# Performance work log

Hardware: AMD Instinct MI355X
Metric: run time of the kernel (lower is better)

The kernel has to match this reference:

```python
import jax, jax.numpy as jnp
import numpy as np

N_NODES = 100000
N_EDGES = 1600000
IN_DIM = 128
OUT_DIM = 32
HEADS = 4
EDGE_DIM = 32
N_ETYPES = 8
NEG_SLOPE = 0.2


def setup_inputs() -> dict:
    key = jax.random.key(0)
    ks = jax.random.split(key, 12)
    return {
        "h": jax.random.normal(ks[0], (N_NODES, IN_DIM), jnp.float32),
        "row": jax.random.randint(ks[1], (N_EDGES,), 0, N_NODES),
        "col": jax.random.randint(ks[2], (N_EDGES,), 0, N_NODES),
        "etype": jax.random.randint(ks[3], (N_EDGES,), 0, N_ETYPES),
        "edge_emb": jax.random.normal(ks[4], (N_ETYPES, EDGE_DIM), jnp.float32),
        "W": jax.random.normal(ks[5], (IN_DIM, OUT_DIM * HEADS), jnp.float32) * 0.1,
        "W_r_w": jax.random.normal(ks[6], (N_ETYPES, EDGE_DIM, EDGE_DIM * HEADS), jnp.float32) * 0.1,
        "a_l": jax.random.normal(ks[7], (1, HEADS, OUT_DIM), jnp.float32) * 0.1,
        "a_r": jax.random.normal(ks[8], (1, HEADS, OUT_DIM), jnp.float32) * 0.1,
        "a_e": jax.random.normal(ks[9], (1, HEADS, EDGE_DIM), jnp.float32) * 0.1,
        "res_w": jax.random.normal(ks[10], (IN_DIM, OUT_DIM * HEADS), jnp.float32) * 0.1,
        "res_b": jax.random.normal(ks[11], (OUT_DIM * HEADS,), jnp.float32) * 0.1,
    }


def reference(h, row, col, etype, edge_emb, W, W_r_w, a_l, a_r, a_e, res_w, res_b):
    N = h.shape[0]
    # node projection: (N, heads, out_dim)
    emb = (h @ W).reshape(N, HEADS, OUT_DIM)
    # TypedLinear on per-etype embeddings: compute once per etype, gather per edge
    typed = jnp.einsum('te,teo->to', edge_emb, W_r_w).reshape(N_ETYPES, HEADS, EDGE_DIM)
    e_emb = typed[etype]                                   # (E, heads, edge_dim)
    # attention logits
    h_l = jnp.sum(a_l * emb, axis=-1)                      # (N, heads)
    h_r = jnp.sum(a_r * emb, axis=-1)                      # (N, heads)
    h_e = jnp.sum(a_e * e_emb, axis=-1)                    # (E, heads)
    logits = jax.nn.leaky_relu(h_l[row] + h_r[col] + h_e, NEG_SLOPE)
    # edge softmax over incoming edges of each destination node (col)
    m = jax.ops.segment_max(logits, col, num_segments=N)   # (N, heads)
    ex = jnp.exp(logits - m[col])
    den = jax.ops.segment_sum(ex, col, num_segments=N)
    alpha = ex / den[col]                                  # (E, heads)
    # weighted scatter-sum aggregation: u_mul_e + sum onto dst
    msg = emb[row] * alpha[:, :, None]                     # (E, heads, out_dim)
    agg = jax.ops.segment_sum(msg, col, num_segments=N)    # (N, heads, out_dim)
    # original permutes emb to (N, out_dim, heads) before flattening
    h_out = jnp.transpose(agg, (0, 2, 1)).reshape(N, OUT_DIM * HEADS)
    h_out = h_out + h @ res_w + res_b                      # residual
    return jax.nn.elu(h_out)
```

## Files before the change

kernel.cpp:

```cpp
#include <hip/hip_runtime.h>

#define NNODES 100000
#define NEDGES 1600000
#define INDIM 128
#define OUTD 32
#define HEADS 4
#define EDIM 32
#define NET 8
#define NEG 0.2f
#define CAP 64
#define RB 392
#define SEGCAP 4608
#define PBLK 196
#define EPB 8192
#define GB2 782

typedef unsigned short u16;
typedef unsigned int u32;
typedef __attribute__((ext_vector_type(8))) short bf16x8;
typedef __attribute__((ext_vector_type(8))) unsigned short ushort8;
typedef __attribute__((ext_vector_type(4))) float f32x4;

__device__ __forceinline__ float bf2f(u16 u){ return __uint_as_float(((u32)u) << 16); }
__device__ __forceinline__ u16 f2bf(float f){
  u32 x = __float_as_uint(f);
  return (u16)((x + 0x7fffu + ((x >> 16) & 1u)) >> 16);
}

__global__ void k_prep(const float* __restrict__ edge_emb, const float* __restrict__ Wr,
                       const float* __restrict__ a_e, const float* __restrict__ W,
                       const float* __restrict__ res_w,
                       float* __restrict__ he_t, u16* __restrict__ Wt,
                       int* __restrict__ cnt, int* __restrict__ gcnt){
  const int b = blockIdx.x, tid = threadIdx.x;
  int4 z4 = make_int4(0, 0, 0, 0);
  for (int i = b * 256 + tid; i < NNODES / 4; i += gridDim.x * 256)
    ((int4*)cnt)[i] = z4;

  if (b == 0){
    for (int t = tid; t < RB; t += 256) gcnt[t] = 0;
    __shared__ float sc[NET * 128];
    for (int idx = tid; idx < NET * 128; idx += 256){
      int t = idx >> 7, o = idx & 127;
      float s = 0.f;
      #pragma unroll
      for (int e = 0; e < EDIM; ++e)
        s += edge_emb[t * EDIM + e] * Wr[t * EDIM * 128 + e * 128 + o];
      sc[idx] = s * a_e[o];
    }
    __syncthreads();
    if (tid < NET * HEADS){
      int t = tid >> 2, h = tid & 3;
      float s = 0.f;
      #pragma unroll
      for (int d = 0; d < EDIM; ++d) s += sc[t * 128 + h * EDIM + d];
      he_t[tid] = s;
    }
  } else {
    int idx = (b - 1) * 256 + tid;
    int n = idx >> 7, k = idx & 127;
    float v = (n < 128) ? W[k * 128 + n] : res_w[k * 128 + (n - 128)];
    Wt[idx] = f2bf(v);
  }
}

__global__ __launch_bounds__(256) void k_fusedA(
    const float* __restrict__ hmat, const u16* __restrict__ Wt,
    const float* __restrict__ res_b, const float* __restrict__ a_l,
    const float* __restrict__ a_r, u16* __restrict__ emb, float* __restrict__ outres,
    float* __restrict__ h_l, float* __restrict__ h_r,
    const int* __restrict__ row, const int* __restrict__ col,
    const int* __restrict__ et, int* __restrict__ gcnt, u32* __restrict__ seg){
  __shared__ u16 rankL[EPB];
  __shared__ int lcnt[RB];
  __shared__ int gbaseL[RB];
  const int tid = threadIdx.x;

  if (blockIdx.x < PBLK){
    for (int t = tid; t < RB; t += 256) lcnt[t] = 0;
    __syncthreads();
    const int base = blockIdx.x * EPB;
    #pragma unroll
    for (int j = 0; j < 8; ++j){
      int e0 = base + j * 1024 + tid * 4;
      if (e0 < NEDGES){
        int4 c4 = *(const int4*)&col[e0];
        int lp = j * 1024 + tid * 4;
        rankL[lp + 0] = (u16)atomicAdd(&lcnt[c4.x >> 8], 1);
        rankL[lp + 1] = (u16)atomicAdd(&lcnt[c4.y >> 8], 1);
        rankL[lp + 2] = (u16)atomicAdd(&lcnt[c4.z >> 8], 1);
        rankL[lp + 3] = (u16)atomicAdd(&lcnt[c4.w >> 8], 1);
      }
    }
    __syncthreads();
    for (int t = tid; t < RB; t += 256){
      int c = lcnt[t];
      gbaseL[t] = (c > 0) ? atomicAdd(&gcnt[t], c) : 0;
    }
    __syncthreads();
    #pragma unroll
    for (int j = 0; j < 8; ++j){
      int e0 = base + j * 1024 + tid * 4;
      if (e0 < NEDGES){
        int4 c4 = *(const int4*)&col[e0];
        int4 r4 = *(const int4*)&row[e0];
        int4 t4 = *(const int4*)&et[e0];
        int lp = j * 1024 + tid * 4;
        int b0 = c4.x >> 8, i0 = gbaseL[b0] + rankL[lp + 0];
        if (i0 < SEGCAP) seg[b0 * SEGCAP + i0] =
            (u32)r4.x | ((u32)t4.x << 17) | ((u32)(c4.x & 255) << 20);
        int b1 = c4.y >> 8, i1 = gbaseL[b1] + rankL[lp + 1];
        if (i1 < SEGCAP) seg[b1 * SEGCAP + i1] =
            (u32)r4.y | ((u32)t4.y << 17) | ((u32)(c4.y & 255) << 20);
        int b2 = c4.z >> 8, i2 = gbaseL[b2] + rankL[lp + 2];
        if (i2 < SEGCAP) seg[b2 * SEGCAP + i2] =
            (u32)r4.z | ((u32)t4.z << 17) | ((u32)(c4.z & 255) << 20);
        int b3 = c4.w >> 8, i3 = gbaseL[b3] + rankL[lp + 3];
        if (i3 < SEGCAP) seg[b3 * SEGCAP + i3] =
            (u32)r4.w | ((u32)t4.w << 17) | ((u32)(c4.w & 255) << 20);
      }
    }
    return;
  }

  const int gb = blockIdx.x - PBLK;
  const int wid = tid >> 6, lane = tid & 63;
  const int m0 = gb * 128 + wid * 32;
  const int mcol = lane & 15, quad = lane >> 4;

  bf16x8 A[2][4];
  #pragma unroll
  for (int mt = 0; mt < 2; ++mt){
    int r = m0 + mt * 16 + mcol;
    int rc = r < NNODES ? r : NNODES - 1;
    const float* hrow = &hmat[rc * 128 + quad * 8];
    #pragma unroll
    for (int ks = 0; ks < 4; ++ks){
      float4 a0 = *(const float4*)&hrow[ks * 32];
      float4 a1 = *(const float4*)&hrow[ks * 32 + 4];
      A[mt][ks][0] = (short)f2bf(a0.x); A[mt][ks][1] = (short)f2bf(a0.y);
      A[mt][ks][2] = (short)f2bf(a0.z); A[mt][ks][3] = (short)f2bf(a0.w);
      A[mt][ks][4] = (short)f2bf(a1.x); A[mt][ks][5] = (short)f2bf(a1.y);
      A[mt][ks][6] = (short)f2bf(a1.z); A[mt][ks][7] = (short)f2bf(a1.w);
    }
  }

  float pl[2][4] = {}, pr[2][4] = {};
  #pragma unroll
  for (int phase = 0; phase < 2; ++phase){
    #pragma unroll
    for (int ntl = 0; ntl < 8; ++ntl){
      bf16x8 B[4];
      const u16* bp = &Wt[(phase * 128 + ntl * 16 + mcol) * 128 + quad * 8];
      #pragma unroll
      for (int ks = 0; ks < 4; ++ks) B[ks] = *(const bf16x8*)&bp[ks * 32];

      f32x4 acc[2] = {{0.f,0.f,0.f,0.f},{0.f,0.f,0.f,0.f}};
      #pragma unroll
      for (int ks = 0; ks < 4; ++ks){
        acc[0] = __builtin_amdgcn_mfma_f32_16x16x32_bf16(A[0][ks], B[ks], acc[0], 0, 0, 0);
        acc[1] = __builtin_amdgcn_mfma_f32_16x16x32_bf16(A[1][ks], B[ks], acc[1], 0, 0, 0);
      }

      const int c = ntl * 16 + mcol;
      if (phase == 0){
        float alc = a_l[c], arc = a_r[c];
        #pragma unroll
        for (int mt = 0; mt < 2; ++mt){
          #pragma unroll
          for (int reg = 0; reg < 4; ++reg){
            int rw = m0 + mt * 16 + quad * 4 + reg;
            if (rw < NNODES) emb[rw * 128 + c] = f2bf(acc[mt][reg]);
            pl[mt][reg] += alc * acc[mt][reg];
            pr[mt][reg] += arc * acc[mt][reg];
          }
        }
        if (ntl & 1){
          int h = ntl >> 1;
          #pragma unroll
          for (int mt = 0; mt < 2; ++mt){
            #pragma unroll
            for (int reg = 0; reg < 4; ++reg){
              float s0 = pl[mt][reg], s1 = pr[mt][reg];
              #pragma unroll
              for (int off = 1; off < 16; off <<= 1){
                s0 += __shfl_xor(s0, off, 64);
                s1 += __shfl_xor(s1, off, 64);
              }
              int rw = m0 + mt * 16 + quad * 4 + reg;
              if (mcol == 0 && rw < NNODES){
                h_l[rw * 4 + h] = s0;
                h_r[rw * 4 + h] = s1;
              }
              pl[mt][reg] = 0.f; pr[mt][reg] = 0.f;
            }
          }
        }
      } else {
        float rb = res_b[c];
        #pragma unroll
        for (int mt = 0; mt < 2; ++mt){
          #pragma unroll
          for (int reg = 0; reg < 4; ++reg){
            int rw = m0 + mt * 16 + quad * 4 + reg;
            if (rw < NNODES) outres[rw * 128 + c] = acc[mt][reg] + rb;
          }
        }
      }
    }
  }
}

__global__ __launch_bounds__(256) void k_bucket(const int* __restrict__ gcnt,
    const u32* __restrict__ seg, int* __restrict__ cnt, int* __restrict__ rtp){
  __shared__ int lc[256];
  const int b = blockIdx.x;
  const int tid = threadIdx.x;
  lc[tid] = 0;
  __syncthreads();
  int m = gcnt[b]; if (m > SEGCAP) m = SEGCAP;
  const u32* s = &seg[b * SEGCAP];
  const int nbase = b << 8;
  for (int i = tid; i < m; i += 256){
    u32 e = s[i];
    int cl = e >> 20;
    int pos = atomicAdd(&lc[cl], 1);
    if (pos < CAP) rtp[(nbase + cl) * CAP + pos] = (int)(e & 0xFFFFFu);
  }
  __syncthreads();
  int node = nbase + tid;
  if (node < NNODES) cnt[node] = lc[tid];
}

__global__ __launch_bounds__(256) void k_nodeagg(const int* __restrict__ cnt,
    const int* __restrict__ rtp, const float* __restrict__ h_l,
    const float* __restrict__ h_r, const float* __restrict__ he_t_g,
    const u16* __restrict__ emb, float* __restrict__ out){
  __shared__ float wl[4][CAP][4];
  __shared__ int   rl[4][CAP];

  const int wid = threadIdx.x >> 6;
  const int n = blockIdx.x * 4 + wid;
  const int lane = threadIdx.x & 63;
  int deg = cnt[n]; if (deg > CAP) deg = CAP;
  const int base = n * CAP;

  {
    bool v = lane < deg;
    int rt = rtp[base + (v ? lane : 0)];
    int r = rt & 0x1FFFF, t = (rt >> 17) & 7;
    float4 hl = *(const float4*)&h_l[r * 4];
    float4 hr = *(const float4*)&h_r[n * 4];
    float4 he = *(const float4*)&he_t_g[t * 4];
    float x0 = hl.x + hr.x + he.x; x0 = x0 > 0.f ? x0 : NEG * x0;
    float x1 = hl.y + hr.y + he.y; x1 = x1 > 0.f ? x1 : NEG * x1;
    float x2 = hl.z + hr.z + he.z; x2 = x2 > 0.f ? x2 : NEG * x2;
    float x3 = hl.w + hr.w + he.w; x3 = x3 > 0.f ? x3 : NEG * x3;
    float4 w4 = make_float4(__expf(x0), __expf(x1), __expf(x2), __expf(x3));
    *(float4*)&wl[wid][lane][0] = w4;
    rl[wid][lane] = r;
  }
  __syncthreads();

  const int q = lane >> 4;
  const int L = lane & 15;
  const int h = L >> 2;

  float acc[8] = {0.f,0.f,0.f,0.f,0.f,0.f,0.f,0.f};
  float ds = 0.f;
  for (int i = 0; i < deg; i += 16){
    int i0 = i + q, i1 = i + 4 + q, i2 = i + 8 + q, i3 = i + 12 + q;
    bool v0 = i0 < deg, v1 = i1 < deg, v2 = i2 < deg, v3 = i3 < deg;
    int ii0 = v0 ? i0 : 0, ii1 = v1 ? i1 : 0;
    int ii2 = v2 ? i2 : 0, ii3 = v3 ? i3 : 0;
    int r0 = rl[wid][ii0];
    int r1 = rl[wid][ii1];
    int r2 = rl[wid][ii2];
    int r3 = rl[wid][ii3];
    float w0 = v0 ? wl[wid][ii0][h] : 0.f;
    float w1 = v1 ? wl[wid][ii1][h] : 0.f;
    float w2 = v2 ? wl[wid][ii2][h] : 0.f;
    float w3 = v3 ? wl[wid][ii3][h] : 0.f;
    ushort8 u0 = *(const ushort8*)&emb[r0 * 128 + L * 8];
    ushort8 u1 = *(const ushort8*)&emb[r1 * 128 + L * 8];
    ushort8 u2 = *(const ushort8*)&emb[r2 * 128 + L * 8];
    ushort8 u3 = *(const ushort8*)&emb[r3 * 128 + L * 8];
    #pragma unroll
    for (int k = 0; k < 8; ++k) acc[k] += w0 * bf2f((u16)u0[k]);
    ds += w0;
    #pragma unroll
    for (int k = 0; k < 8; ++k) acc[k] += w1 * bf2f((u16)u1[k]);
    ds += w1;
    #pragma unroll
    for (int k = 0; k < 8; ++k) acc[k] += w2 * bf2f((u16)u2[k]);
    ds += w2;
    #pragma unroll
    for (int k = 0; k < 8; ++k) acc[k] += w3 * bf2f((u16)u3[k]);
    ds += w3;
  }

  #pragma unroll
  for (int k = 0; k < 8; ++k){
    acc[k] += __shfl_xor(acc[k], 16, 64);
    acc[k] += __shfl_xor(acc[k], 32, 64);
  }
  ds += __shfl_xor(ds, 16, 64);
  ds += __shfl_xor(ds, 32, 64);

  if (q == 0){
    float inv = (deg > 0) ? 1.f / ds : 0.f;
    int ob = n * 128 + (L & 3) * 32 + (L >> 2);
    #pragma unroll
    for (int k = 0; k < 8; ++k){
      int o = ob + k * 4;
      float v = acc[k] * inv + out[o];
      out[o] = v > 0.f ? v : (__expf(v) - 1.f);
    }
  }
}

extern "C" void kernel_launch(void* const* d_in, const int* in_sizes, int n_in,
                              void* d_out, int out_size, void* d_ws, size_t ws_size,
                              hipStream_t stream){
  const float* hmat     = (const float*)d_in[0];
  const int*   row      = (const int*)d_in[1];
  const int*   col      = (const int*)d_in[2];
  const int*   et       = (const int*)d_in[3];
  const float* edge_emb = (const float*)d_in[4];
  const float* W        = (const float*)d_in[5];
  const float* Wr       = (const float*)d_in[6];
  const float* a_l      = (const float*)d_in[7];
  const float* a_r      = (const float*)d_in[8];
  const float* a_e      = (const float*)d_in[9];
  const float* res_w    = (const float*)d_in[10];
  const float* res_b    = (const float*)d_in[11];
  float* out = (float*)d_out;

  char* ws = (char*)d_ws;
  float* he_t   = (float*)(ws);
  u16*   Wt     = (u16*)  (ws + 256);
  float* h_l    = (float*)(ws + 65792);
  float* h_r    = (float*)(ws + 1665792);
  int*   cnt    = (int*)  (ws + 3265792);
  int*   gcnt   = (int*)  (ws + 3665792);
  u32*   seg    = (u32*)  (ws + 3667360);
  int*   rtp    = (int*)  (ws + 10892704);
  u16*   emb    = (u16*)  (ws + 36492704);

  hipLaunchKernelGGL(k_prep, dim3(129), dim3(256), 0, stream,
                     edge_emb, Wr, a_e, W, res_w, he_t, Wt, cnt, gcnt);
  hipLaunchKernelGGL(k_fusedA, dim3(PBLK + GB2), dim3(256), 0, stream,
                     hmat, Wt, res_b, a_l, a_r, emb, out, h_l, h_r,
                     row, col, et, gcnt, seg);
  hipLaunchKernelGGL(k_bucket, dim3(RB), dim3(256), 0, stream,
                     gcnt, seg, cnt, rtp);
  hipLaunchKernelGGL(k_nodeagg, dim3(NNODES / 4), dim3(256), 0, stream,
                     cnt, rtp, h_l, h_r, he_t, emb, out);
}
```

Measured before the change: 303.5 us.

## Regroup kernels: fuse prep with edge partition, fuse GEMM with bucketing

The kernels are regrouped so that weight and edge-type prep run as extra blocks alongside the coarse edge partitioning, and the per-bucket node sort runs as extra blocks alongside the node GEMM. The global bucket counters are now cleared with a memset instead of inside the prep kernel. This removes one kernel launch and lets independent work overlap within a launch. The cnt zeroing moves away, since the bucket stage writes every node count. The partitioning kernel now carries extra shared memory for the prep block, which may lower occupancy.

```diff
diff --git a/kernel.cpp b/kernel.cpp
--- a/kernel.cpp
+++ b/kernel.cpp
@@ -27,59 +27,24 @@
   return (u16)((x + 0x7fffu + ((x >> 16) & 1u)) >> 16);
 }
 
-__global__ void k_prep(const float* __restrict__ edge_emb, const float* __restrict__ Wr,
-                       const float* __restrict__ a_e, const float* __restrict__ W,
-                       const float* __restrict__ res_w,
-                       float* __restrict__ he_t, u16* __restrict__ Wt,
-                       int* __restrict__ cnt, int* __restrict__ gcnt){
-  const int b = blockIdx.x, tid = threadIdx.x;
-  int4 z4 = make_int4(0, 0, 0, 0);
-  for (int i = b * 256 + tid; i < NNODES / 4; i += gridDim.x * 256)
-    ((int4*)cnt)[i] = z4;
-
-  if (b == 0){
-    for (int t = tid; t < RB; t += 256) gcnt[t] = 0;
-    __shared__ float sc[NET * 128];
-    for (int idx = tid; idx < NET * 128; idx += 256){
-      int t = idx >> 7, o = idx & 127;
-      float s = 0.f;
-      #pragma unroll
-      for (int e = 0; e < EDIM; ++e)
-        s += edge_emb[t * EDIM + e] * Wr[t * EDIM * 128 + e * 128 + o];
-      sc[idx] = s * a_e[o];
-    }
-    __syncthreads();
-    if (tid < NET * HEADS){
-      int t = tid >> 2, h = tid & 3;
-      float s = 0.f;
-      #pragma unroll
-      for (int d = 0; d < EDIM; ++d) s += sc[t * 128 + h * EDIM + d];
-      he_t[tid] = s;
-    }
-  } else {
-    int idx = (b - 1) * 256 + tid;
-    int n = idx >> 7, k = idx & 127;
-    float v = (n < 128) ? W[k * 128 + n] : res_w[k * 128 + (n - 128)];
-    Wt[idx] = f2bf(v);
-  }
-}
-
-__global__ __launch_bounds__(256) void k_fusedA(
-    const float* __restrict__ hmat, const u16* __restrict__ Wt,
-    const float* __restrict__ res_b, const float* __restrict__ a_l,
-    const float* __restrict__ a_r, u16* __restrict__ emb, float* __restrict__ outres,
-    float* __restrict__ h_l, float* __restrict__ h_r,
+__global__ __launch_bounds__(256) void k_prepart(
+    const float* __restrict__ edge_emb, const float* __restrict__ Wr,
+    const float* __restrict__ a_e, const float* __restrict__ W,
+    const float* __restrict__ res_w, float* __restrict__ he_t,
+    u16* __restrict__ Wt,
     const int* __restrict__ row, const int* __restrict__ col,
     const int* __restrict__ et, int* __restrict__ gcnt, u32* __restrict__ seg){
   __shared__ u16 rankL[EPB];
   __shared__ int lcnt[RB];
   __shared__ int gbaseL[RB];
+  __shared__ float sc[NET * 128];
   const int tid = threadIdx.x;
-
-  if (blockIdx.x < PBLK){
+  const int b = blockIdx.x;
+
+  if (b < PBLK){
     for (int t = tid; t < RB; t += 256) lcnt[t] = 0;
     __syncthreads();
-    const int base = blockIdx.x * EPB;
+    const int base = b * EPB;
     #pragma unroll
     for (int j = 0; j < 8; ++j){
       int e0 = base + j * 1024 + tid * 4;
@@ -120,10 +85,61 @@
             (u32)r4.w | ((u32)t4.w << 17) | ((u32)(c4.w & 255) << 20);
       }
     }
+  } else if (b == PBLK){
+    for (int idx = tid; idx < NET * 128; idx += 256){
+      int t = idx >> 7, o = idx & 127;
+      float s = 0.f;
+      #pragma unroll
+      for (int e = 0; e < EDIM; ++e)
+        s += edge_emb[t * EDIM + e] * Wr[t * EDIM * 128 + e * 128 + o];
+      sc[idx] = s * a_e[o];
+    }
+    __syncthreads();
+    if (tid < NET * HEADS){
+      int t = tid >> 2, h = tid & 3;
+      float s = 0.f;
+      #pragma unroll
+      for (int d = 0; d < EDIM; ++d) s += sc[t * 128 + h * EDIM + d];
+      he_t[tid] = s;
+    }
+  } else {
+    int idx = (b - PBLK - 1) * 256 + tid;
+    int n = idx >> 7, k = idx & 127;
+    float v = (n < 128) ? W[k * 128 + n] : res_w[k * 128 + (n - 128)];
+    Wt[idx] = f2bf(v);
+  }
+}
+
+__global__ __launch_bounds__(256) void k_gemmbucket(
+    const float* __restrict__ hmat, const u16* __restrict__ Wt,
+    const float* __restrict__ res_b, const float* __restrict__ a_l,
+    const float* __restrict__ a_r, u16* __restrict__ emb, float* __restrict__ outres,
+    float* __restrict__ h_l, float* __restrict__ h_r,
+    const int* __restrict__ gcnt, const u32* __restrict__ seg,
+    int* __restrict__ cnt, int* __restrict__ rtp){
+  __shared__ int lc[256];
+  const int tid = threadIdx.x;
+
+  if (blockIdx.x < RB){
+    const int b = blockIdx.x;
+    lc[tid] = 0;
+    __syncthreads();
+    int m = gcnt[b]; if (m > SEGCAP) m = SEGCAP;
+    const u32* s = &seg[b * SEGCAP];
+    const int nbase = b << 8;
+    for (int i = tid; i < m; i += 256){
+      u32 e = s[i];
+      int cl = e >> 20;
+      int pos = atomicAdd(&lc[cl], 1);
+      if (pos < CAP) rtp[(nbase + cl) * CAP + pos] = (int)(e & 0xFFFFFu);
+    }
+    __syncthreads();
+    int node = nbase + tid;
+    if (node < NNODES) cnt[node] = lc[tid];
     return;
   }
 
-  const int gb = blockIdx.x - PBLK;
+  const int gb = blockIdx.x - RB;
   const int wid = tid >> 6, lane = tid & 63;
   const int m0 = gb * 128 + wid * 32;
   const int mcol = lane & 15, quad = lane >> 4;
@@ -211,27 +227,6 @@
   }
 }
 
-__global__ __launch_bounds__(256) void k_bucket(const int* __restrict__ gcnt,
-    const u32* __restrict__ seg, int* __restrict__ cnt, int* __restrict__ rtp){
-  __shared__ int lc[256];
-  const int b = blockIdx.x;
-  const int tid = threadIdx.x;
-  lc[tid] = 0;
-  __syncthreads();
-  int m = gcnt[b]; if (m > SEGCAP) m = SEGCAP;
-  const u32* s = &seg[b * SEGCAP];
-  const int nbase = b << 8;
-  for (int i = tid; i < m; i += 256){
-    u32 e = s[i];
-    int cl = e >> 20;
-    int pos = atomicAdd(&lc[cl], 1);
-    if (pos < CAP) rtp[(nbase + cl) * CAP + pos] = (int)(e & 0xFFFFFu);
-  }
-  __syncthreads();
-  int node = nbase + tid;
-  if (node < NNODES) cnt[node] = lc[tid];
-}
-
 __global__ __launch_bounds__(256) void k_nodeagg(const int* __restrict__ cnt,
     const int* __restrict__ rtp, const float* __restrict__ h_l,
     const float* __restrict__ h_r, const float* __restrict__ he_t_g,
@@ -347,12 +342,12 @@
   int*   rtp    = (int*)  (ws + 10892704);
   u16*   emb    = (u16*)  (ws + 36492704);
 
-  hipLaunchKernelGGL(k_prep, dim3(129), dim3(256), 0, stream,
-                     edge_emb, Wr, a_e, W, res_w, he_t, Wt, cnt, gcnt);
-  hipLaunchKernelGGL(k_fusedA, dim3(PBLK + GB2), dim3(256), 0, stream,
+  hipMemsetAsync(gcnt, 0, RB * sizeof(int), stream);
+  hipLaunchKernelGGL(k_prepart, dim3(PBLK + 129), dim3(256), 0, stream,
+                     edge_emb, Wr, a_e, W, res_w, he_t, Wt,
+                     row, col, et, gcnt, seg);
+  hipLaunchKernelGGL(k_gemmbucket, dim3(RB + GB2), dim3(256), 0, stream,
                      hmat, Wt, res_b, a_l, a_r, emb, out, h_l, h_r,
-                     row, col, et, gcnt, seg);
-  hipLaunchKernelGGL(k_bucket, dim3(RB), dim3(256), 0, stream,
                      gcnt, seg, cnt, rtp);
   hipLaunchKernelGGL(k_nodeagg, dim3(NNODES / 4), dim3(256), 0, stream,
                      cnt, rtp, h_l, h_r, he_t, emb, out);
```

Measured after the change: 306.0 us. Within noise of the previous version (+0.8%).
